# Kernel optimization log

Hardware: AMD Instinct MI355X
Metric: run time of the kernel (lower is better)

The kernel has to match this reference:

```python
import jax, jax.numpy as jnp
import numpy as np

B, L, E, H, V, ENC = 64, 51, 512, 512, 30000, 2048


def setup_inputs() -> dict:
    key = jax.random.key(0)
    ks = jax.random.split(key, 12)
    encoder_out = jax.random.normal(ks[0], (B, ENC), jnp.float32)
    encoded_captions = jax.random.randint(ks[1], (B, L), 0, V)
    lengths = jax.random.randint(ks[2], (B,), 2, L + 1)
    lengths = lengths.at[0].set(L)  # ensure max(decode_lengths) == L-1 so T is static
    caption_lengths = lengths[:, None]

    def lin(k, out_d, in_d):
        bnd = 1.0 / np.sqrt(in_d)
        kw, kb = jax.random.split(k)
        w = jax.random.uniform(kw, (out_d, in_d), jnp.float32, -bnd, bnd)
        b = jax.random.uniform(kb, (out_d,), jnp.float32, -bnd, bnd)
        return w, b

    embedding_weight = jax.random.uniform(ks[3], (V, E), jnp.float32, -0.1, 0.1)
    w_ih, b_ih = lin(ks[4], 4 * H, E)
    w_hh, b_hh = lin(ks[5], 4 * H, H)
    w_init_h, b_init_h = lin(ks[6], H, ENC)
    w_init_c, b_init_c = lin(ks[7], H, ENC)
    w_fc = jax.random.uniform(ks[8], (V, H), jnp.float32, -0.1, 0.1)
    b_fc = jnp.zeros((V,), jnp.float32)
    return dict(encoder_out=encoder_out, encoded_captions=encoded_captions,
                caption_lengths=caption_lengths, embedding_weight=embedding_weight,
                w_ih=w_ih, b_ih=b_ih, w_hh=w_hh, b_hh=b_hh,
                w_init_h=w_init_h, b_init_h=b_init_h,
                w_init_c=w_init_c, b_init_c=b_init_c, w_fc=w_fc, b_fc=b_fc)


def _forward(encoder_out, embedding_weight, w_ih, b_ih, w_hh, b_hh,
             w_init_h, b_init_h, w_init_c, b_init_c, w_fc, b_fc,
             encoded_captions, caption_lengths):
    lengths = caption_lengths[:, 0]
    sort_ind = jnp.argsort(-lengths)          # descending-length sort
    enc = encoder_out[sort_ind]
    caps = encoded_captions[sort_ind]
    dec_len = lengths[sort_ind] - 1           # [B]
    embs = embedding_weight[caps]             # [B, L, E]
    h0 = enc @ w_init_h.T + b_init_h          # [B, H]
    c0 = enc @ w_init_c.T + b_init_c
    T = caps.shape[1] - 1                     # static max(decode_lengths)
    xs = (jnp.transpose(embs[:, :T], (1, 0, 2)), jnp.arange(T))

    # Note: the torch loop trims h,c to batch_size_t; because lengths are
    # sorted descending, trimmed rows never produce outputs again, so running
    # the full batch and masking finished rows yields identical predictions.
    def step(carry, xt):
        h, c = carry
        x, t = xt
        gates = x @ w_ih.T + b_ih + h @ w_hh.T + b_hh   # [B, 4H]
        i, f, g, o = jnp.split(gates, 4, axis=-1)       # LSTMCell gate order
        c = jax.nn.sigmoid(f) * c + jax.nn.sigmoid(i) * jnp.tanh(g)
        h = jax.nn.sigmoid(o) * jnp.tanh(c)
        preds = h @ w_fc.T + b_fc                        # dropout = identity (eval)
        preds = jnp.where((t < dec_len)[:, None], preds, 0.0)
        return (h, c), preds

    _, preds = jax.lax.scan(step, (h0, c0), xs)          # [T, B, V]
    predictions = jnp.transpose(preds, (1, 0, 2))        # [B, T, V]
    return predictions, caps, dec_len, sort_ind


def reference(encoder_out, encoded_captions, caption_lengths, embedding_weight,
              w_ih, b_ih, w_hh, b_hh, w_init_h, b_init_h, w_init_c, b_init_c,
              w_fc, b_fc):
    return _forward(encoder_out, embedding_weight, w_ih, b_ih, w_hh, b_hh,
                    w_init_h, b_init_h, w_init_c, b_init_c, w_fc, b_fc,
                    encoded_captions, caption_lengths)
```

## Files before the change

kernel.cpp:

```cpp
#include <hip/hip_runtime.h>

#define NB    64
#define LCAP  51
#define TT    50
#define HID   512
#define EMB   512
#define VOC   30000
#define ENCD  2048
#define G4    2048

typedef unsigned short u16;
typedef unsigned int   u32;
typedef __attribute__((ext_vector_type(8))) short bf16x8;
typedef __attribute__((ext_vector_type(4))) float f32x4;
typedef __attribute__((ext_vector_type(4))) unsigned int u32x4;

__device__ __forceinline__ u16 f2bf(float x) {
  union { float f; unsigned u; } v; v.f = x;
  unsigned r = v.u + 0x7fffu + ((v.u >> 16) & 1u);
  return (u16)(r >> 16);
}

__device__ __forceinline__ float fast_sigmoid(float x) {
  return 1.f / (1.f + __expf(-x));
}
__device__ __forceinline__ float fast_tanh(float x) {
  float xx = fminf(fmaxf(x, -10.f), 10.f);
  float e = __expf(2.f * xx);
  return (e - 1.f) * __frcp_rn(e + 1.f);
}

__global__ __launch_bounds__(256) void sort_k(const int* __restrict__ cap_len,
                                              const int* __restrict__ caps,
                                              float* __restrict__ out,
                                              int* __restrict__ sind,
                                              int* __restrict__ dlen,
                                              int* __restrict__ rowmap,
                                              int* __restrict__ zmap,
                                              int* __restrict__ nact,
                                              int* __restrict__ flags) {
  __shared__ int smlen[NB];
  __shared__ int smpos[NB];
  __shared__ int sdl[NB];
  __shared__ int off[NB];
  __shared__ int zoff[NB];
  int tid = threadIdx.x;
  if (tid < NB) { smlen[tid] = cap_len[tid]; flags[tid] = 0; }
  __syncthreads();
  if (tid < NB) {
    int li = smlen[tid];
    int rank = 0;
    for (int j = 0; j < NB; ++j) {
      int lj = smlen[j];
      rank += (lj > li || (lj == li && j < tid)) ? 1 : 0;
    }
    smpos[rank] = tid;
  }
  __syncthreads();
  if (tid < NB) {
    int src = smpos[tid];
    int dl = smlen[src] - 1;
    sind[tid] = src;
    dlen[tid] = dl;
    sdl[tid] = dl;
    float* caps_out = out + (size_t)NB * TT * VOC;
    for (int l = 0; l < LCAP; ++l)
      caps_out[tid * LCAP + l] = (float)caps[src * LCAP + l];
    out[96003264 + tid] = (float)dl;
    out[96003328 + tid] = (float)src;
  }
  __syncthreads();
  if (tid == 0) {
    int s = 0, z = 0;
    for (int b = 0; b < NB; ++b) {
      off[b] = s;  s += sdl[b];
      zoff[b] = z; z += TT - sdl[b];
    }
    *nact = s;
  }
  __syncthreads();
  for (int m = tid; m < NB * TT; m += 256) {
    int b = (m * 5243) >> 18;
    int t = m - b * TT;
    if (t < sdl[b]) rowmap[off[b] + t] = m;
    else            zmap[zoff[b] + (t - sdl[b])] = m;
  }
}

__global__ __launch_bounds__(256) void conv4(const float* __restrict__ src,
                                             u16* __restrict__ dst, int n4) {
  int i = blockIdx.x * 256 + threadIdx.x;
  if (i >= n4) return;
  float4 v = ((const float4*)src)[i];
  ushort4 o;
  o.x = f2bf(v.x); o.y = f2bf(v.y); o.z = f2bf(v.z); o.w = f2bf(v.w);
  ((ushort4*)dst)[i] = o;
}

__global__ __launch_bounds__(256) void conv_winit_k(const float* __restrict__ wh,
                                                    const float* __restrict__ wc,
                                                    u16* __restrict__ dst) {
  int i = blockIdx.x * 256 + threadIdx.x;
  if (i >= 524288) return;
  int e = i * 4;
  int row = e >> 11;
  int col = e & 2047;
  const float* src = (row < 512) ? (wh + (size_t)row * 2048 + col)
                                 : (wc + (size_t)(row - 512) * 2048 + col);
  float4 v = *(const float4*)src;
  ushort4 o;
  o.x = f2bf(v.x); o.y = f2bf(v.y); o.z = f2bf(v.z); o.w = f2bf(v.w);
  ((ushort4*)dst)[i] = o;
}

__global__ __launch_bounds__(256) void gather_enc_k(const float* __restrict__ enc,
                                                    const int* __restrict__ sind,
                                                    u16* __restrict__ dst) {
  int i = blockIdx.x * 256 + threadIdx.x;
  if (i >= 32768) return;
  int e = i * 4;
  int r = e >> 11;
  int k = e & 2047;
  float4 v = *(const float4*)(enc + (size_t)sind[r] * ENCD + k);
  ushort4 o;
  o.x = f2bf(v.x); o.y = f2bf(v.y); o.z = f2bf(v.z); o.w = f2bf(v.w);
  ((ushort4*)dst)[i] = o;
}

__global__ __launch_bounds__(256) void gather_x_k(const float* __restrict__ emb,
                                                  const int* __restrict__ caps,
                                                  const int* __restrict__ sind,
                                                  u16* __restrict__ dst) {
  int i = blockIdx.x * 256 + threadIdx.x;
  if (i >= 409600) return;
  int e = i * 4;
  int m = e >> 9;
  int k = e & 511;
  unsigned b = ((unsigned)m * 5243u) >> 18;
  int t = m - (int)b * TT;
  int cap = caps[sind[b] * LCAP + t];
  float4 v = *(const float4*)(emb + (size_t)cap * EMB + k);
  ushort4 o;
  o.x = f2bf(v.x); o.y = f2bf(v.y); o.z = f2bf(v.z); o.w = f2bf(v.w);
  ((ushort4*)dst)[i] = o;
}

#define BM 128
#define BN 128
#define BK 32
#define LDT 40

template <int EPI>
__global__ __launch_bounds__(256) void gemm_bt(const u16* __restrict__ A,
                                               const u16* __restrict__ Bm,
                                               int Mr, int Nr, int K,
                                               void* __restrict__ outv,
                                               float* __restrict__ out1,
                                               const float* __restrict__ bias0,
                                               const float* __restrict__ bias1,
                                               const int* __restrict__ rowmap,
                                               const int* __restrict__ zmap,
                                               const int* __restrict__ nactp) {
  __shared__ u16 As[BM * LDT];
  __shared__ u16 Bs[BN * LDT];
  __shared__ int rmap_s[BM];
  int tid = threadIdx.x;
  int mBase = blockIdx.x * BM;
  int nBase = blockIdx.y * BN;
  int nact = Mr;

  if (EPI == 2) {
    nact = nactp[0];
    int nz = Mr - nact;
    if (tid < 32 && nz > 0) {
      int nc4 = min(BN, Nr - nBase) >> 2;
      float4 zz = {0.f, 0.f, 0.f, 0.f};
      if (tid < nc4) {
        for (int r = blockIdx.x; r < nz; r += gridDim.x) {
          float4* dst = (float4*)((float*)outv + (size_t)zmap[r] * Nr + nBase);
          dst[tid] = zz;
        }
      }
    }
    int na = (nact + BM - 1) >> 7;
    if ((int)blockIdx.x >= na) return;
    if (tid < BM) {
      int idx = mBase + tid;
      rmap_s[tid] = (idx < nact) ? rowmap[idx] : rowmap[nact - 1];
    }
    __syncthreads();
  }

  int wid = tid >> 6, lane = tid & 63;
  int wm = (wid >> 1) * 64, wn = (wid & 1) * 64;
  int lm = lane & 15, lq = lane >> 4;

  f32x4 acc[4][4];
  for (int i = 0; i < 4; ++i)
    for (int j = 0; j < 4; ++j)
      acc[i][j] = (f32x4){0.f, 0.f, 0.f, 0.f};

  int nkt = K / BK;
  for (int kt = 0; kt < nkt; ++kt) {
    for (int it = 0; it < 2; ++it) {
      int li = tid + it * 256;
      int row = li >> 2, kq = li & 3;
      {
        int gr = (EPI == 2) ? rmap_s[row] : min(mBase + row, Mr - 1);
        uint4 v = *(const uint4*)(A + (size_t)gr * K + kt * BK + kq * 8);
        *(uint4*)&As[row * LDT + kq * 8] = v;
      }
      {
        int gr = min(nBase + row, Nr - 1);
        uint4 v = *(const uint4*)(Bm + (size_t)gr * K + kt * BK + kq * 8);
        *(uint4*)&Bs[row * LDT + kq * 8] = v;
      }
    }
    __syncthreads();
    bf16x8 af[4], bfr[4];
    for (int i = 0; i < 4; ++i)
      af[i] = *(const bf16x8*)&As[(wm + i * 16 + lm) * LDT + lq * 8];
    for (int j = 0; j < 4; ++j)
      bfr[j] = *(const bf16x8*)&Bs[(wn + j * 16 + lm) * LDT + lq * 8];
    for (int i = 0; i < 4; ++i)
      for (int j = 0; j < 4; ++j)
        acc[i][j] = __builtin_amdgcn_mfma_f32_16x16x32_bf16(af[i], bfr[j], acc[i][j], 0, 0, 0);
    __syncthreads();
  }

  for (int i = 0; i < 4; ++i) {
    int rloc0 = wm + i * 16 + (lane >> 4) * 4;
    for (int j = 0; j < 4; ++j) {
      int col = nBase + wn + j * 16 + (lane & 15);
      for (int r = 0; r < 4; ++r) {
        int rloc = rloc0 + r;
        float v = acc[i][j][r];
        if (EPI == 0) {
          int row = mBase + rloc;
          if (row < Mr && col < Nr)
            ((float*)outv)[(size_t)row * Nr + col] = v + bias0[col] + bias1[col];
        } else if (EPI == 1) {
          int row = mBase + rloc;
          if (row < Mr && col < Nr) {
            if (col < 512) {
              int jj = col >> 3;
              ((u16*)outv)[(size_t)jj * 512 + row * 8 + (col & 7)] = f2bf(v + bias0[col]);
            } else {
              out1[(size_t)row * 512 + (col - 512)] = v + bias1[col - 512];
            }
          }
        } else {
          if (col < Nr && mBase + rloc < nact)
            ((float*)outv)[(size_t)rmap_s[rloc] * Nr + col] = v + bias0[col];
        }
      }
    }
  }
}

__global__ __launch_bounds__(256, 1) void lstm_seq(const float* __restrict__ w_hh,
                                                   const float* __restrict__ xW,
                                                   const float* __restrict__ cbuf,
                                                   u32* __restrict__ hx,
                                                   u32* __restrict__ Hs32,
                                                   int* __restrict__ flg) {
  __shared__ u16 wsm[32 * 520];
  __shared__ float gsm[64][36];
  __shared__ u32 hsh[256];
  int tid = threadIdx.x;
  int j = blockIdx.x;
  int u0 = j * 8;

  {
    int r = tid >> 3;
    int cc = (tid & 7) * 64;
    const float* src = w_hh + (size_t)((r >> 3) * HID + u0 + (r & 7)) * HID + cc;
    u16* dst = &wsm[r * 520 + cc];
#pragma unroll
    for (int q = 0; q < 16; ++q) {
      float4 v = ((const float4*)src)[q];
      ushort4 o; o.x = f2bf(v.x); o.y = f2bf(v.y); o.z = f2bf(v.z); o.w = f2bf(v.w);
      ((ushort4*)dst)[q] = o;
    }
  }
  __syncthreads();

  int wave = tid >> 6, lane = tid & 63;
  int lm = lane & 15, lq = lane >> 4;

  bf16x8 bfrag[2][16];
#pragma unroll
  for (int n = 0; n < 2; ++n)
#pragma unroll
    for (int kq = 0; kq < 16; ++kq)
      bfrag[n][kq] = *(const bf16x8*)&wsm[(n * 16 + lm) * 520 + kq * 32 + lq * 8];

  int b = tid >> 2, up = tid & 3;
  float creg[2];
  {
    float2 c2 = *(const float2*)&cbuf[(size_t)b * HID + u0 + 2 * up];
    creg[0] = c2.x; creg[1] = c2.y;
  }

  const int abase = lq * 256 + (wave * 16 + lm) * 4;

  for (int t = 0; t < TT; ++t) {
    const u32* hcur = hx + (size_t)(t & 1) * (NB * 256);
    u32* hnxt = hx + (size_t)((t + 1) & 1) * (NB * 256);

    float xg[4][2];
    {
      const float* xwp = xW + (size_t)(b * TT + t) * G4 + u0 + 2 * up;
#pragma unroll
      for (int g = 0; g < 4; ++g) {
        float2 v = *(const float2*)&xwp[g * HID];
        xg[g][0] = v.x; xg[g][1] = v.y;
      }
    }

    if (t > 0) {
      if (wave == 0 && lane < 16) {
        const u32* myp = (const u32*)flg + lane;
        u32 f;
        u32 tt = (u32)t;
        for (;;) {
          asm volatile("global_load_dword %0, %1, off sc0 sc1"
                       : "=v"(f) : "v"(myp) : "memory");
          asm volatile("s_waitcnt vmcnt(0)" : "+v"(f) :: "memory");
          if (((f & 0xffu) >= tt) & (((f >> 8) & 0xffu) >= tt) &
              (((f >> 16) & 0xffu) >= tt) & ((f >> 24) >= tt)) break;
          __builtin_amdgcn_s_sleep(1);
        }
      }
      __syncthreads();
    }

    u32x4 raw[16];
#pragma unroll
    for (int kq = 0; kq < 16; ++kq) {
      const u32* p = hcur + abase + kq * 1024;
      asm volatile("global_load_dwordx4 %0, %1, off sc0 sc1"
                   : "=v"(raw[kq]) : "v"(p) : "memory");
    }
    asm volatile("s_waitcnt vmcnt(0)"
                 : "+v"(raw[0]), "+v"(raw[1]), "+v"(raw[2]), "+v"(raw[3]),
                   "+v"(raw[4]), "+v"(raw[5]), "+v"(raw[6]), "+v"(raw[7]),
                   "+v"(raw[8]), "+v"(raw[9]), "+v"(raw[10]), "+v"(raw[11]),
                   "+v"(raw[12]), "+v"(raw[13]), "+v"(raw[14]), "+v"(raw[15])
                 :: "memory");

    f32x4 acc0 = (f32x4){0.f, 0.f, 0.f, 0.f};
    f32x4 acc1 = (f32x4){0.f, 0.f, 0.f, 0.f};
#pragma unroll
    for (int kq = 0; kq < 16; ++kq) {
      bf16x8 a = __builtin_bit_cast(bf16x8, raw[kq]);
      acc0 = __builtin_amdgcn_mfma_f32_16x16x32_bf16(a, bfrag[0][kq], acc0, 0, 0, 0);
      acc1 = __builtin_amdgcn_mfma_f32_16x16x32_bf16(a, bfrag[1][kq], acc1, 0, 0, 0);
    }
#pragma unroll
    for (int r = 0; r < 4; ++r) {
      gsm[wave * 16 + lq * 4 + r][lm]      = acc0[r];
      gsm[wave * 16 + lq * 4 + r][16 + lm] = acc1[r];
    }

    float hn2[2];
#pragma unroll
    for (int e = 0; e < 2; ++e) {
      int ul = 2 * up + e;
      float gi = gsm[b][ul]      + xg[0][e];
      float gf = gsm[b][8 + ul]  + xg[1][e];
      float gg = gsm[b][16 + ul] + xg[2][e];
      float go = gsm[b][24 + ul] + xg[3][e];
      float cn = fast_sigmoid(gf) * creg[e] + fast_sigmoid(gi) * fast_tanh(gg);
      creg[e] = cn;
      hn2[e] = fast_sigmoid(go) * fast_tanh(cn);
    }
    hsh[b * 4 + up] = (u32)f2bf(hn2[0]) | ((u32)f2bf(hn2[1]) << 16);
    __syncthreads();

    if (tid < 64) {
      u32x4 hv = *(const u32x4*)&hsh[tid * 4];
      u32* dst = hnxt + j * 256 + tid * 4;
      asm volatile("global_store_dwordx4 %0, %1, off sc0 sc1"
                   :: "v"(dst), "v"(hv) : "memory");
      asm volatile("s_waitcnt vmcnt(0)" ::: "memory");
      if (tid == 0) {
        u32 fv = (u32)(t + 1);
        unsigned char* fj = (unsigned char*)flg + j;
        asm volatile("global_store_byte %0, %1, off sc0 sc1"
                     :: "v"(fj), "v"(fv) : "memory");
      }
      *(u32x4*)(Hs32 + ((size_t)tid * TT + t) * 256 + j * 4) = hv;
    }
  }
}

extern "C" void kernel_launch(void* const* d_in, const int* in_sizes, int n_in,
                              void* d_out, int out_size, void* d_ws, size_t ws_size,
                              hipStream_t stream) {
  const float* encoder_out = (const float*)d_in[0];
  const int*   caps        = (const int*)d_in[1];
  const int*   cap_len     = (const int*)d_in[2];
  const float* emb         = (const float*)d_in[3];
  const float* w_ih        = (const float*)d_in[4];
  const float* b_ih        = (const float*)d_in[5];
  const float* w_hh        = (const float*)d_in[6];
  const float* b_hh        = (const float*)d_in[7];
  const float* w_init_h    = (const float*)d_in[8];
  const float* b_init_h    = (const float*)d_in[9];
  const float* w_init_c    = (const float*)d_in[10];
  const float* b_init_c    = (const float*)d_in[11];
  const float* w_fc        = (const float*)d_in[12];
  const float* b_fc        = (const float*)d_in[13];
  float* out = (float*)d_out;

  char* ws = (char*)d_ws;
  int*   sind   = (int*)(ws + 0);
  int*   dlen   = (int*)(ws + 256);
  int*   nact   = (int*)(ws + 512);
  int*   flags  = (int*)(ws + 576);
  int*   rowmap = (int*)(ws + 832);
  int*   zmap   = (int*)(ws + 13632);
  float* cbuf   = (float*)(ws + 26496);
  u16*   hbuf   = (u16*)(ws + 157568);
  float* xW     = (float*)(ws + 288640);
  u16*   Hs     = (u16*)(ws + 26503040);
  u16*   Xb     = (u16*)(ws + 29779840);
  u16*   Wih    = (u16*)(ws + 33056640);
  u16*   Winit  = (u16*)(ws + 35153792);
  u16*   Wfc    = (u16*)(ws + 39348096);
  u16*   Ebf    = (u16*)(ws + 70068096);

  sort_k<<<1, 256, 0, stream>>>(cap_len, caps, out, sind, dlen, rowmap, zmap, nact, flags);
  conv4<<<1024, 256, 0, stream>>>(w_ih, Wih, 262144);
  conv_winit_k<<<2048, 256, 0, stream>>>(w_init_h, w_init_c, Winit);
  conv4<<<15000, 256, 0, stream>>>(w_fc, Wfc, 3840000);
  gather_enc_k<<<128, 256, 0, stream>>>(encoder_out, sind, Ebf);
  gather_x_k<<<1600, 256, 0, stream>>>(emb, caps, sind, Xb);

  gemm_bt<1><<<dim3(1, 8), 256, 0, stream>>>(Ebf, Winit, 64, 1024, 2048,
                                             hbuf, cbuf, b_init_h, b_init_c,
                                             nullptr, nullptr, nullptr);
  gemm_bt<0><<<dim3(25, 16), 256, 0, stream>>>(Xb, Wih, 3200, 2048, 512,
                                               xW, nullptr, b_ih, b_hh,
                                               nullptr, nullptr, nullptr);
  lstm_seq<<<64, 256, 0, stream>>>(w_hh, xW, cbuf, (u32*)hbuf, (u32*)Hs, flags);
  gemm_bt<2><<<dim3(25, 235), 256, 0, stream>>>(Hs, Wfc, 3200, VOC, 512,
                                                out, nullptr, b_fc, nullptr,
                                                rowmap, zmap, nact);
}
```

Before: 957.4 us.

## Fuse LSTM recurrence with output FC GEMM via flag-based producer/consumer overlap

Merges the sequential LSTM kernel and the vocabulary projection GEMM into one persistent launch. 64 blocks run the recurrence while 192 blocks consume completed timestep pairs, polling the per-block step flags before computing the FC tiles. The compact active-row remapping is dropped: every row is computed and finished rows are masked to zero in the epilogue. This hides the large FC GEMM behind the latency-bound recurrence, but it computes masked rows it used to skip and adds spin-polling and a deadlock risk if the blocks are not all co-resident.

Measured after the change: 1.043 ms. 9.0% more time.

```diff
diff --git a/kernel.cpp b/kernel.cpp
--- a/kernel.cpp
+++ b/kernel.cpp
@@ -30,20 +30,29 @@
   return (e - 1.f) * __frcp_rn(e + 1.f);
 }
 
+__device__ __forceinline__ void poll_flags16(const int* flg, int lane, u32 tt) {
+  if (lane < 16) {
+    const u32* myp = (const u32*)flg + lane;
+    u32 f;
+    for (;;) {
+      asm volatile("global_load_dword %0, %1, off sc0 sc1"
+                   : "=v"(f) : "v"(myp) : "memory");
+      asm volatile("s_waitcnt vmcnt(0)" : "+v"(f) :: "memory");
+      if (((f & 0xffu) >= tt) & (((f >> 8) & 0xffu) >= tt) &
+          (((f >> 16) & 0xffu) >= tt) & ((f >> 24) >= tt)) break;
+      __builtin_amdgcn_s_sleep(1);
+    }
+  }
+}
+
 __global__ __launch_bounds__(256) void sort_k(const int* __restrict__ cap_len,
                                               const int* __restrict__ caps,
                                               float* __restrict__ out,
                                               int* __restrict__ sind,
                                               int* __restrict__ dlen,
-                                              int* __restrict__ rowmap,
-                                              int* __restrict__ zmap,
-                                              int* __restrict__ nact,
                                               int* __restrict__ flags) {
   __shared__ int smlen[NB];
   __shared__ int smpos[NB];
-  __shared__ int sdl[NB];
-  __shared__ int off[NB];
-  __shared__ int zoff[NB];
   int tid = threadIdx.x;
   if (tid < NB) { smlen[tid] = cap_len[tid]; flags[tid] = 0; }
   __syncthreads();
@@ -62,28 +71,11 @@
     int dl = smlen[src] - 1;
     sind[tid] = src;
     dlen[tid] = dl;
-    sdl[tid] = dl;
     float* caps_out = out + (size_t)NB * TT * VOC;
     for (int l = 0; l < LCAP; ++l)
       caps_out[tid * LCAP + l] = (float)caps[src * LCAP + l];
     out[96003264 + tid] = (float)dl;
     out[96003328 + tid] = (float)src;
-  }
-  __syncthreads();
-  if (tid == 0) {
-    int s = 0, z = 0;
-    for (int b = 0; b < NB; ++b) {
-      off[b] = s;  s += sdl[b];
-      zoff[b] = z; z += TT - sdl[b];
-    }
-    *nact = s;
-  }
-  __syncthreads();
-  for (int m = tid; m < NB * TT; m += 256) {
-    int b = (m * 5243) >> 18;
-    int t = m - b * TT;
-    if (t < sdl[b]) rowmap[off[b] + t] = m;
-    else            zmap[zoff[b] + (t - sdl[b])] = m;
   }
 }
 
@@ -157,39 +149,12 @@
                                                void* __restrict__ outv,
                                                float* __restrict__ out1,
                                                const float* __restrict__ bias0,
-                                               const float* __restrict__ bias1,
-                                               const int* __restrict__ rowmap,
-                                               const int* __restrict__ zmap,
-                                               const int* __restrict__ nactp) {
+                                               const float* __restrict__ bias1) {
   __shared__ u16 As[BM * LDT];
   __shared__ u16 Bs[BN * LDT];
-  __shared__ int rmap_s[BM];
   int tid = threadIdx.x;
   int mBase = blockIdx.x * BM;
   int nBase = blockIdx.y * BN;
-  int nact = Mr;
-
-  if (EPI == 2) {
-    nact = nactp[0];
-    int nz = Mr - nact;
-    if (tid < 32 && nz > 0) {
-      int nc4 = min(BN, Nr - nBase) >> 2;
-      float4 zz = {0.f, 0.f, 0.f, 0.f};
-      if (tid < nc4) {
-        for (int r = blockIdx.x; r < nz; r += gridDim.x) {
-          float4* dst = (float4*)((float*)outv + (size_t)zmap[r] * Nr + nBase);
-          dst[tid] = zz;
-        }
-      }
-    }
-    int na = (nact + BM - 1) >> 7;
-    if ((int)blockIdx.x >= na) return;
-    if (tid < BM) {
-      int idx = mBase + tid;
-      rmap_s[tid] = (idx < nact) ? rowmap[idx] : rowmap[nact - 1];
-    }
-    __syncthreads();
-  }
 
   int wid = tid >> 6, lane = tid & 63;
   int wm = (wid >> 1) * 64, wn = (wid & 1) * 64;
@@ -206,7 +171,7 @@
       int li = tid + it * 256;
       int row = li >> 2, kq = li & 3;
       {
-        int gr = (EPI == 2) ? rmap_s[row] : min(mBase + row, Mr - 1);
+        int gr = min(mBase + row, Mr - 1);
         uint4 v = *(const uint4*)(A + (size_t)gr * K + kt * BK + kq * 8);
         *(uint4*)&As[row * LDT + kq * 8] = v;
       }
@@ -239,7 +204,7 @@
           int row = mBase + rloc;
           if (row < Mr && col < Nr)
             ((float*)outv)[(size_t)row * Nr + col] = v + bias0[col] + bias1[col];
-        } else if (EPI == 1) {
+        } else {
           int row = mBase + rloc;
           if (row < Mr && col < Nr) {
             if (col < 512) {
@@ -249,148 +214,229 @@
               out1[(size_t)row * 512 + (col - 512)] = v + bias1[col - 512];
             }
           }
-        } else {
-          if (col < Nr && mBase + rloc < nact)
-            ((float*)outv)[(size_t)rmap_s[rloc] * Nr + col] = v + bias0[col];
         }
       }
     }
   }
 }
 
-__global__ __launch_bounds__(256, 1) void lstm_seq(const float* __restrict__ w_hh,
-                                                   const float* __restrict__ xW,
-                                                   const float* __restrict__ cbuf,
-                                                   u32* __restrict__ hx,
-                                                   u32* __restrict__ Hs32,
-                                                   int* __restrict__ flg) {
-  __shared__ u16 wsm[32 * 520];
-  __shared__ float gsm[64][36];
-  __shared__ u32 hsh[256];
+__global__ __launch_bounds__(256, 1) void lstm_fc(const float* __restrict__ w_hh,
+                                                  const float* __restrict__ xW,
+                                                  const float* __restrict__ cbuf,
+                                                  u32* __restrict__ hx,
+                                                  u32* __restrict__ Hs32,
+                                                  int* __restrict__ flg,
+                                                  const u16* __restrict__ Wfc,
+                                                  const float* __restrict__ b_fc,
+                                                  const int* __restrict__ dlen,
+                                                  float* __restrict__ out) {
+  __shared__ __align__(16) char smem[43520];
   int tid = threadIdx.x;
-  int j = blockIdx.x;
-  int u0 = j * 8;
-
-  {
-    int r = tid >> 3;
-    int cc = (tid & 7) * 64;
-    const float* src = w_hh + (size_t)((r >> 3) * HID + u0 + (r & 7)) * HID + cc;
-    u16* dst = &wsm[r * 520 + cc];
-#pragma unroll
-    for (int q = 0; q < 16; ++q) {
-      float4 v = ((const float4*)src)[q];
-      ushort4 o; o.x = f2bf(v.x); o.y = f2bf(v.y); o.z = f2bf(v.z); o.w = f2bf(v.w);
-      ((ushort4*)dst)[q] = o;
-    }
-  }
-  __syncthreads();
-
   int wave = tid >> 6, lane = tid & 63;
   int lm = lane & 15, lq = lane >> 4;
 
-  bf16x8 bfrag[2][16];
-#pragma unroll
-  for (int n = 0; n < 2; ++n)
-#pragma unroll
-    for (int kq = 0; kq < 16; ++kq)
-      bfrag[n][kq] = *(const bf16x8*)&wsm[(n * 16 + lm) * 520 + kq * 32 + lq * 8];
-
-  int b = tid >> 2, up = tid & 3;
-  float creg[2];
-  {
-    float2 c2 = *(const float2*)&cbuf[(size_t)b * HID + u0 + 2 * up];
-    creg[0] = c2.x; creg[1] = c2.y;
-  }
-
-  const int abase = lq * 256 + (wave * 16 + lm) * 4;
-
-  for (int t = 0; t < TT; ++t) {
-    const u32* hcur = hx + (size_t)(t & 1) * (NB * 256);
-    u32* hnxt = hx + (size_t)((t + 1) & 1) * (NB * 256);
-
-    float xg[4][2];
+  if (blockIdx.x < 64) {
+    u16* wsm = (u16*)smem;
+    float* gsmf = (float*)(smem + 33280);
+    u32* hsh = (u32*)(smem + 33280 + 9216);
+#define GSM(rr, cc) gsmf[(rr) * 36 + (cc)]
+    int j = blockIdx.x;
+    int u0 = j * 8;
+
     {
-      const float* xwp = xW + (size_t)(b * TT + t) * G4 + u0 + 2 * up;
-#pragma unroll
-      for (int g = 0; g < 4; ++g) {
-        float2 v = *(const float2*)&xwp[g * HID];
-        xg[g][0] = v.x; xg[g][1] = v.y;
-      }
-    }
-
-    if (t > 0) {
-      if (wave == 0 && lane < 16) {
-        const u32* myp = (const u32*)flg + lane;
-        u32 f;
-        u32 tt = (u32)t;
-        for (;;) {
-          asm volatile("global_load_dword %0, %1, off sc0 sc1"
-                       : "=v"(f) : "v"(myp) : "memory");
-          asm volatile("s_waitcnt vmcnt(0)" : "+v"(f) :: "memory");
-          if (((f & 0xffu) >= tt) & (((f >> 8) & 0xffu) >= tt) &
-              (((f >> 16) & 0xffu) >= tt) & ((f >> 24) >= tt)) break;
-          __builtin_amdgcn_s_sleep(1);
+      int r = tid >> 3;
+      int cc = (tid & 7) * 64;
+      const float* src = w_hh + (size_t)((r >> 3) * HID + u0 + (r & 7)) * HID + cc;
+      u16* dst = &wsm[r * 520 + cc];
+#pragma unroll
+      for (int q = 0; q < 16; ++q) {
+        float4 v = ((const float4*)src)[q];
+        ushort4 o; o.x = f2bf(v.x); o.y = f2bf(v.y); o.z = f2bf(v.z); o.w = f2bf(v.w);
+        ((ushort4*)dst)[q] = o;
+      }
+    }
+    __syncthreads();
+
+    bf16x8 bfrag[2][16];
+#pragma unroll
+    for (int n = 0; n < 2; ++n)
+#pragma unroll
+      for (int kq = 0; kq < 16; ++kq)
+        bfrag[n][kq] = *(const bf16x8*)&wsm[(n * 16 + lm) * 520 + kq * 32 + lq * 8];
+
+    int b = tid >> 2, up = tid & 3;
+    float creg[2];
+    {
+      float2 c2 = *(const float2*)&cbuf[(size_t)b * HID + u0 + 2 * up];
+      creg[0] = c2.x; creg[1] = c2.y;
+    }
+
+    const int abase = lq * 256 + (wave * 16 + lm) * 4;
+
+    for (int t = 0; t < TT; ++t) {
+      const u32* hcur = hx + (size_t)(t & 1) * (NB * 256);
+      u32* hnxt = hx + (size_t)((t + 1) & 1) * (NB * 256);
+
+      float xg[4][2];
+      {
+        const float* xwp = xW + (size_t)(b * TT + t) * G4 + u0 + 2 * up;
+#pragma unroll
+        for (int g = 0; g < 4; ++g) {
+          float2 v = *(const float2*)&xwp[g * HID];
+          xg[g][0] = v.x; xg[g][1] = v.y;
         }
       }
+
+      if (t > 0) {
+        if (wave == 0) poll_flags16(flg, lane, (u32)t);
+        __syncthreads();
+      }
+
+      u32x4 raw[16];
+#pragma unroll
+      for (int kq = 0; kq < 16; ++kq) {
+        const u32* p = hcur + abase + kq * 1024;
+        asm volatile("global_load_dwordx4 %0, %1, off sc0 sc1"
+                     : "=v"(raw[kq]) : "v"(p) : "memory");
+      }
+      asm volatile("s_waitcnt vmcnt(0)"
+                   : "+v"(raw[0]), "+v"(raw[1]), "+v"(raw[2]), "+v"(raw[3]),
+                     "+v"(raw[4]), "+v"(raw[5]), "+v"(raw[6]), "+v"(raw[7]),
+                     "+v"(raw[8]), "+v"(raw[9]), "+v"(raw[10]), "+v"(raw[11]),
+                     "+v"(raw[12]), "+v"(raw[13]), "+v"(raw[14]), "+v"(raw[15])
+                   :: "memory");
+
+      f32x4 acc0 = (f32x4){0.f, 0.f, 0.f, 0.f};
+      f32x4 acc1 = (f32x4){0.f, 0.f, 0.f, 0.f};
+#pragma unroll
+      for (int kq = 0; kq < 16; ++kq) {
+        bf16x8 a = __builtin_bit_cast(bf16x8, raw[kq]);
+        acc0 = __builtin_amdgcn_mfma_f32_16x16x32_bf16(a, bfrag[0][kq], acc0, 0, 0, 0);
+        acc1 = __builtin_amdgcn_mfma_f32_16x16x32_bf16(a, bfrag[1][kq], acc1, 0, 0, 0);
+      }
+#pragma unroll
+      for (int r = 0; r < 4; ++r) {
+        GSM(wave * 16 + lq * 4 + r, lm)      = acc0[r];
+        GSM(wave * 16 + lq * 4 + r, 16 + lm) = acc1[r];
+      }
+
+      float hn2[2];
+#pragma unroll
+      for (int e = 0; e < 2; ++e) {
+        int ul = 2 * up + e;
+        float gi = GSM(b, ul)      + xg[0][e];
+        float gf = GSM(b, 8 + ul)  + xg[1][e];
+        float gg = GSM(b, 16 + ul) + xg[2][e];
+        float go = GSM(b, 24 + ul) + xg[3][e];
+        float cn = fast_sigmoid(gf) * creg[e] + fast_sigmoid(gi) * fast_tanh(gg);
+        creg[e] = cn;
+        hn2[e] = fast_sigmoid(go) * fast_tanh(cn);
+      }
+      hsh[b * 4 + up] = (u32)f2bf(hn2[0]) | ((u32)f2bf(hn2[1]) << 16);
       __syncthreads();
-    }
-
-    u32x4 raw[16];
-#pragma unroll
-    for (int kq = 0; kq < 16; ++kq) {
-      const u32* p = hcur + abase + kq * 1024;
-      asm volatile("global_load_dwordx4 %0, %1, off sc0 sc1"
-                   : "=v"(raw[kq]) : "v"(p) : "memory");
-    }
-    asm volatile("s_waitcnt vmcnt(0)"
-                 : "+v"(raw[0]), "+v"(raw[1]), "+v"(raw[2]), "+v"(raw[3]),
-                   "+v"(raw[4]), "+v"(raw[5]), "+v"(raw[6]), "+v"(raw[7]),
-                   "+v"(raw[8]), "+v"(raw[9]), "+v"(raw[10]), "+v"(raw[11]),
-                   "+v"(raw[12]), "+v"(raw[13]), "+v"(raw[14]), "+v"(raw[15])
-                 :: "memory");
-
-    f32x4 acc0 = (f32x4){0.f, 0.f, 0.f, 0.f};
-    f32x4 acc1 = (f32x4){0.f, 0.f, 0.f, 0.f};
-#pragma unroll
-    for (int kq = 0; kq < 16; ++kq) {
-      bf16x8 a = __builtin_bit_cast(bf16x8, raw[kq]);
-      acc0 = __builtin_amdgcn_mfma_f32_16x16x32_bf16(a, bfrag[0][kq], acc0, 0, 0, 0);
-      acc1 = __builtin_amdgcn_mfma_f32_16x16x32_bf16(a, bfrag[1][kq], acc1, 0, 0, 0);
-    }
-#pragma unroll
-    for (int r = 0; r < 4; ++r) {
-      gsm[wave * 16 + lq * 4 + r][lm]      = acc0[r];
-      gsm[wave * 16 + lq * 4 + r][16 + lm] = acc1[r];
-    }
-
-    float hn2[2];
-#pragma unroll
-    for (int e = 0; e < 2; ++e) {
-      int ul = 2 * up + e;
-      float gi = gsm[b][ul]      + xg[0][e];
-      float gf = gsm[b][8 + ul]  + xg[1][e];
-      float gg = gsm[b][16 + ul] + xg[2][e];
-      float go = gsm[b][24 + ul] + xg[3][e];
-      float cn = fast_sigmoid(gf) * creg[e] + fast_sigmoid(gi) * fast_tanh(gg);
-      creg[e] = cn;
-      hn2[e] = fast_sigmoid(go) * fast_tanh(cn);
-    }
-    hsh[b * 4 + up] = (u32)f2bf(hn2[0]) | ((u32)f2bf(hn2[1]) << 16);
-    __syncthreads();
-
-    if (tid < 64) {
-      u32x4 hv = *(const u32x4*)&hsh[tid * 4];
-      u32* dst = hnxt + j * 256 + tid * 4;
-      asm volatile("global_store_dwordx4 %0, %1, off sc0 sc1"
-                   :: "v"(dst), "v"(hv) : "memory");
+
+      if (tid < 64) {
+        u32x4 hv = *(const u32x4*)&hsh[tid * 4];
+        u32* dst = hnxt + j * 256 + tid * 4;
+        asm volatile("global_store_dwordx4 %0, %1, off sc0 sc1"
+                     :: "v"(dst), "v"(hv) : "memory");
+        asm volatile("s_waitcnt vmcnt(0)" ::: "memory");
+        if (tid == 0) {
+          u32 fv = (u32)(t + 1);
+          unsigned char* fj = (unsigned char*)flg + j;
+          asm volatile("global_store_byte %0, %1, off sc0 sc1"
+                       :: "v"(fj), "v"(fv) : "memory");
+        }
+        u32* hdst = Hs32 + ((size_t)tid * TT + t) * 256 + j * 4;
+        asm volatile("global_store_dwordx4 %0, %1, off sc0 sc1"
+                     :: "v"(hdst), "v"(hv) : "memory");
+      }
+    }
+    if (wave == 0) {
       asm volatile("s_waitcnt vmcnt(0)" ::: "memory");
-      if (tid == 0) {
-        u32 fv = (u32)(t + 1);
+      if (lane == 0) {
+        u32 fv = 51u;
         unsigned char* fj = (unsigned char*)flg + j;
         asm volatile("global_store_byte %0, %1, off sc0 sc1"
                      :: "v"(fj), "v"(fv) : "memory");
       }
-      *(u32x4*)(Hs32 + ((size_t)tid * TT + t) * 256 + j * 4) = hv;
+    }
+#undef GSM
+  } else {
+    u16* As = (u16*)smem;
+    u16* Bs = (u16*)(smem + 10240);
+    int* dl_s = (int*)(smem + 20480);
+    const u16* HsA = (const u16*)Hs32;
+
+    if (tid < NB) dl_s[tid] = dlen[tid];
+
+    const int F = 192;
+    int f = blockIdx.x - 64;
+    int wid = wave;
+    int wm = (wid >> 1) * 64, wn = (wid & 1) * 64;
+
+    int lastNeed = 0;
+    for (int tile = f; tile < 25 * 235; tile += F) {
+      int t2 = tile / 235;
+      int nb = tile - t2 * 235;
+      int t0 = t2 * 2;
+      int nBase = nb * 128;
+      int need = (t0 == 48) ? 51 : (t0 + 3);
+      if (need > lastNeed) {
+        if (wid == 0) poll_flags16(flg, lane, (u32)need);
+        lastNeed = need;
+      }
+      __syncthreads();
+
+      f32x4 acc[4][4];
+      for (int i = 0; i < 4; ++i)
+        for (int jj = 0; jj < 4; ++jj)
+          acc[i][jj] = (f32x4){0.f, 0.f, 0.f, 0.f};
+
+      for (int kt = 0; kt < 16; ++kt) {
+        for (int it = 0; it < 2; ++it) {
+          int li = tid + it * 256;
+          int row = li >> 2, kq = li & 3;
+          {
+            int gr = (row & 63) * TT + t0 + (row >> 6);
+            uint4 v = *(const uint4*)(HsA + (size_t)gr * 512 + kt * BK + kq * 8);
+            *(uint4*)&As[row * LDT + kq * 8] = v;
+          }
+          {
+            int gb = min(nBase + row, VOC - 1);
+            uint4 v = *(const uint4*)(Wfc + (size_t)gb * 512 + kt * BK + kq * 8);
+            *(uint4*)&Bs[row * LDT + kq * 8] = v;
+          }
+        }
+        __syncthreads();
+        bf16x8 af[4], bfr[4];
+        for (int i = 0; i < 4; ++i)
+          af[i] = *(const bf16x8*)&As[(wm + i * 16 + lm) * LDT + lq * 8];
+        for (int jj = 0; jj < 4; ++jj)
+          bfr[jj] = *(const bf16x8*)&Bs[(wn + jj * 16 + lm) * LDT + lq * 8];
+        for (int i = 0; i < 4; ++i)
+          for (int jj = 0; jj < 4; ++jj)
+            acc[i][jj] = __builtin_amdgcn_mfma_f32_16x16x32_bf16(af[i], bfr[jj], acc[i][jj], 0, 0, 0);
+        __syncthreads();
+      }
+
+      for (int i = 0; i < 4; ++i) {
+        int rloc0 = wm + i * 16 + lq * 4;
+        for (int jj = 0; jj < 4; ++jj) {
+          int col = nBase + wn + jj * 16 + lm;
+          if (col < VOC) {
+            float bias = b_fc[col];
+            for (int r = 0; r < 4; ++r) {
+              int rloc = rloc0 + r;
+              int bb = rloc & 63;
+              int tcur = t0 + (rloc >> 6);
+              float v = acc[i][jj][r] + bias;
+              float o = (tcur < dl_s[bb]) ? v : 0.f;
+              out[(size_t)(bb * TT + tcur) * VOC + col] = o;
+            }
+          }
+        }
+      }
     }
   }
 }
@@ -419,8 +465,6 @@
   int*   dlen   = (int*)(ws + 256);
   int*   nact   = (int*)(ws + 512);
   int*   flags  = (int*)(ws + 576);
-  int*   rowmap = (int*)(ws + 832);
-  int*   zmap   = (int*)(ws + 13632);
   float* cbuf   = (float*)(ws + 26496);
   u16*   hbuf   = (u16*)(ws + 157568);
   float* xW     = (float*)(ws + 288640);
@@ -430,8 +474,9 @@
   u16*   Winit  = (u16*)(ws + 35153792);
   u16*   Wfc    = (u16*)(ws + 39348096);
   u16*   Ebf    = (u16*)(ws + 70068096);
-
-  sort_k<<<1, 256, 0, stream>>>(cap_len, caps, out, sind, dlen, rowmap, zmap, nact, flags);
+  (void)nact;
+
+  sort_k<<<1, 256, 0, stream>>>(cap_len, caps, out, sind, dlen, flags);
   conv4<<<1024, 256, 0, stream>>>(w_ih, Wih, 262144);
   conv_winit_k<<<2048, 256, 0, stream>>>(w_init_h, w_init_c, Winit);
   conv4<<<15000, 256, 0, stream>>>(w_fc, Wfc, 3840000);
@@ -439,13 +484,9 @@
   gather_x_k<<<1600, 256, 0, stream>>>(emb, caps, sind, Xb);
 
   gemm_bt<1><<<dim3(1, 8), 256, 0, stream>>>(Ebf, Winit, 64, 1024, 2048,
-                                             hbuf, cbuf, b_init_h, b_init_c,
-                                             nullptr, nullptr, nullptr);
+                                             hbuf, cbuf, b_init_h, b_init_c);
   gemm_bt<0><<<dim3(25, 16), 256, 0, stream>>>(Xb, Wih, 3200, 2048, 512,
-                                               xW, nullptr, b_ih, b_hh,
-                                               nullptr, nullptr, nullptr);
-  lstm_seq<<<64, 256, 0, stream>>>(w_hh, xW, cbuf, (u32*)hbuf, (u32*)Hs, flags);
-  gemm_bt<2><<<dim3(25, 235), 256, 0, stream>>>(Hs, Wfc, 3200, VOC, 512,
-                                                out, nullptr, b_fc, nullptr,
-                                                rowmap, zmap, nact);
-}
+                                               xW, nullptr, b_ih, b_hh);
+  lstm_fc<<<256, 256, 0, stream>>>(w_hh, xW, cbuf, (u32*)hbuf, (u32*)Hs, flags,
+                                   Wfc, b_fc, dlen, out);
+}
```
